# Performance work log

Measured on AMD Instinct MI355X. Metric: run time of the kernel, lower is better.

## Reference

```python
import jax, jax.numpy as jnp
import numpy as np

BN_EPS = 1e-5

def setup_inputs() -> dict:
    key = jax.random.key(0)
    ks = jax.random.split(key, 7)
    B, D, A = 16384, 768, 51
    s = 1.0 / np.sqrt(D)
    return {
        "x": jax.random.normal(ks[0], (B, D), dtype=jnp.float32),
        "W_embed": jax.random.uniform(ks[1], (D, D), minval=-s, maxval=s, dtype=jnp.float32),
        "b_embed": jax.random.uniform(ks[2], (D,), minval=-s, maxval=s, dtype=jnp.float32),
        "W_attr": jax.random.uniform(ks[3], (A, D), minval=-s, maxval=s, dtype=jnp.float32),  # stacked per-attribute (dim->1) heads
        "b_attr": jax.random.uniform(ks[4], (A,), minval=-s, maxval=s, dtype=jnp.float32),
        "gamma": jnp.ones((A,), dtype=jnp.float32),
        "beta": jnp.zeros((A,), dtype=jnp.float32),
    }

def reference(x, W_embed, b_embed, W_attr, b_attr, gamma, beta):
    # word_embed: Linear(dim, dim)
    h = x @ W_embed.T + b_embed                      # [B, D]
    # fused per-attribute heads: cat of attr_num (dim->1) linears == one (dim->attr_num) matmul
    logits = h @ W_attr.T + b_attr                    # [B, A]
    # BatchNorm1d (training mode: batch statistics, biased variance)
    mean = jnp.mean(logits, axis=0)
    var = jnp.var(logits, axis=0)
    y = (logits - mean) * jax.lax.rsqrt(var + BN_EPS) * gamma + beta
    return y
```

## Files before the change

### kernel.cpp

```cpp
#include <hip/hip_runtime.h>
#include <hip/hip_bf16.h>

typedef _Float16 halfx8 __attribute__((ext_vector_type(8)));
typedef _Float16 halfx4 __attribute__((ext_vector_type(4)));
typedef float floatx4 __attribute__((ext_vector_type(4)));

#define GLOBAL_AS __attribute__((address_space(1)))
#define LDS_AS __attribute__((address_space(3)))

__device__ __forceinline__ void async_copy_16(const void* g, void* l) {
    __builtin_amdgcn_global_load_lds((GLOBAL_AS void*)g, (LDS_AS void*)l, 16, 0, 0);
}

#define PM 16384
#define PD 768
#define PA 51


__global__ __launch_bounds__(256) void init_kernel(
    const float* __restrict__ Wa, const float* __restrict__ b_embed,
    const float* __restrict__ b_attr,
    float* __restrict__ wc32, float* __restrict__ bc, float* __restrict__ stats)
{
    int b = blockIdx.x, t = threadIdx.x;
    if (b < 12) {
        #pragma unroll
        for (int j = 0; j < 4; ++j)
            ((float4*)wc32)[b * 1024 + j * 256 + t] = (float4){0.f, 0.f, 0.f, 0.f};
    } else {
        if (t < 128) stats[t] = 0.f;
        __shared__ float red[256];
        int a = t & 63, qtr = t >> 6;
        float partial = 0.f;
        if (a < PA) {
            const float* war = Wa + (size_t)a * PD + qtr * 192;
            const float* ber = b_embed + qtr * 192;
            #pragma unroll 4
            for (int k = 0; k < 192; k += 4) {
                floatx4 w = *(const floatx4*)(war + k);
                floatx4 e = *(const floatx4*)(ber + k);
                partial += w[0]*e[0] + w[1]*e[1] + w[2]*e[2] + w[3]*e[3];
            }
        }
        red[t] = partial;
        __syncthreads();
        if (t < PA)
            bc[t] = red[t] + red[64 + t] + red[128 + t] + red[192 + t] + b_attr[t];
    }
}

__global__ __launch_bounds__(256) void wcomb_kernel(
    const float* __restrict__ We, const float* __restrict__ Wa,
    float* __restrict__ wc32)
{
    __shared__ float WeS[48 * 64];
    __shared__ float WaS[51 * 48];
    const int b = blockIdx.x;
    const int kc = b & 15;
    const int nc = b >> 4;
    const int k0 = kc * 48, d0 = nc * 64;
    const int t = threadIdx.x;

    #pragma unroll
    for (int j = 0; j < 3; ++j) {
        int idx4 = j * 256 + t;
        int r = idx4 >> 4, c4 = idx4 & 15;
        *(floatx4*)&WeS[r * 64 + c4 * 4] =
            *(const floatx4*)(We + (size_t)(k0 + r) * PD + d0 + c4 * 4);
    }
    for (int idx4 = t; idx4 < 612; idx4 += 256) {
        int r = idx4 / 12, c4 = idx4 % 12;
        *(floatx4*)&WaS[r * 48 + c4 * 4] =
            *(const floatx4*)(Wa + (size_t)r * PD + k0 + c4 * 4);
    }
    __syncthreads();

    const int c = t & 63;
    const int ag = t >> 6;

    float we[48];
    #pragma unroll
    for (int k = 0; k < 48; ++k) we[k] = WeS[k * 64 + c];

    #pragma unroll
    for (int i = 0; i < 13; ++i) {
        int a = ag + i * 4;
        if (a < PA) {
            float acc = 0.f;
            #pragma unroll
            for (int k4 = 0; k4 < 12; ++k4) {
                floatx4 wa = *(const floatx4*)&WaS[a * 48 + k4 * 4];
                acc += wa[0] * we[k4*4] + wa[1] * we[k4*4+1]
                     + wa[2] * we[k4*4+2] + wa[3] * we[k4*4+3];
            }
            atomicAdd(&wc32[(size_t)a * PD + d0 + c], acc);
        }
    }
}

__global__ __launch_bounds__(256) void skinny_gemm_kernel(
    const float* __restrict__ X,
    const float* __restrict__ Wc,
    const float* __restrict__ bc,
    float* __restrict__ logits,
    float* __restrict__ stats)
{
    __shared__ float As[32 * 64];
    __shared__ float Bs[64 * 64];
    __shared__ float s_sum[64];
    __shared__ float s_ssq[64];

    const int tid = threadIdx.x;
    const int wave = tid >> 6;
    const int lane = tid & 63;
    const int quad = lane >> 4;
    const int l16 = lane & 15;
    const int wr = wave & 1;
    const int wn = wave >> 1;
    const int row0 = blockIdx.x * 32;

    if (tid < 64) { s_sum[tid] = 0.f; s_ssq[tid] = 0.f; }

    const int g_r  = lane >> 4;
    const int g_sl = lane & 15;

    floatx4 acc[2];
    acc[0] = (floatx4){0.f, 0.f, 0.f, 0.f};
    acc[1] = (floatx4){0.f, 0.f, 0.f, 0.f};

    for (int kt = 0; kt < PD; kt += 64) {
        #pragma unroll
        for (int j = 0; j < 2; ++j) {
            int g = wave * 2 + j;
            int r = g * 4 + g_r;
            int csrc = g_sl ^ (r & 7);
            async_copy_16(X + (size_t)(row0 + r) * PD + kt + csrc * 4, &As[g * 256]);
        }
        #pragma unroll
        for (int j = 0; j < 4; ++j) {
            int g = wave * 4 + j;
            int r = g * 4 + g_r;
            int csrc = g_sl ^ (r & 7);
            async_copy_16(Wc + (size_t)r * PD + kt + csrc * 4, &Bs[g * 256]);
        }
        __syncthreads();
        #pragma unroll
        for (int ks = 0; ks < 2; ++ks) {
            int c0 = ks * 8 + quad * 2;
            int sw = l16 & 7;
            int rA = wr * 16 + l16;
            floatx4 p0 = *(const floatx4*)&As[rA * 64 + ((c0 ^ sw) << 2)];
            floatx4 p1 = *(const floatx4*)&As[rA * 64 + (((c0 + 1) ^ sw) << 2)];
            halfx8 af;
            af[0] = (_Float16)p0[0]; af[1] = (_Float16)p0[1];
            af[2] = (_Float16)p0[2]; af[3] = (_Float16)p0[3];
            af[4] = (_Float16)p1[0]; af[5] = (_Float16)p1[1];
            af[6] = (_Float16)p1[2]; af[7] = (_Float16)p1[3];
            #pragma unroll
            for (int ni = 0; ni < 2; ++ni) {
                int rB = wn * 32 + ni * 16 + l16;
                floatx4 q0 = *(const floatx4*)&Bs[rB * 64 + ((c0 ^ sw) << 2)];
                floatx4 q1 = *(const floatx4*)&Bs[rB * 64 + (((c0 + 1) ^ sw) << 2)];
                halfx8 bf;
                bf[0] = (_Float16)q0[0]; bf[1] = (_Float16)q0[1];
                bf[2] = (_Float16)q0[2]; bf[3] = (_Float16)q0[3];
                bf[4] = (_Float16)q1[0]; bf[5] = (_Float16)q1[1];
                bf[6] = (_Float16)q1[2]; bf[7] = (_Float16)q1[3];
                acc[ni] = __builtin_amdgcn_mfma_f32_16x16x32_f16(af, bf, acc[ni], 0, 0, 0);
            }
        }
        __syncthreads();
    }

    #pragma unroll
    for (int ni = 0; ni < 2; ++ni) {
        int col = wn * 32 + ni * 16 + l16;
        if (col < PA) {
            float bv = bc[col];
            float ps = 0.f, pss = 0.f;
            int rowb = row0 + wr * 16 + quad * 4;
            #pragma unroll
            for (int r = 0; r < 4; ++r) {
                float v = acc[ni][r] + bv;
                logits[(size_t)(rowb + r) * PA + col] = v;
                ps += v; pss += v * v;
            }
            atomicAdd(&s_sum[col], ps);
            atomicAdd(&s_ssq[col], pss);
        }
    }
    __syncthreads();
    if (tid < PA) {
        atomicAdd(&stats[tid], s_sum[tid]);
        atomicAdd(&stats[64 + tid], s_ssq[tid]);
    }
}

__global__ void bn_finalize_kernel(const float* __restrict__ logits,
                                   const float* __restrict__ stats,
                                   const float* __restrict__ gamma,
                                   const float* __restrict__ beta,
                                   float* __restrict__ out, int total) {
    __shared__ float s_scale[PA];
    __shared__ float s_shift[PA];
    int t = threadIdx.x;
    if (t < PA) {
        const float invB = 1.0f / (float)PM;
        float mean = stats[t] * invB;
        float var = stats[64 + t] * invB - mean * mean;
        float inv = rsqrtf(var + 1e-5f);
        float g = gamma[t] * inv;
        s_scale[t] = g;
        s_shift[t] = beta[t] - mean * g;
    }
    __syncthreads();
    int idx = blockIdx.x * 256 + t;
    if (idx < total) {
        int col = idx % PA;
        out[idx] = logits[idx] * s_scale[col] + s_shift[col];
    }
}

extern "C" void kernel_launch(void* const* d_in, const int* in_sizes, int n_in,
                              void* d_out, int out_size, void* d_ws, size_t ws_size,
                              hipStream_t stream) {
    const float* x       = (const float*)d_in[0];
    const float* W_embed = (const float*)d_in[1];
    const float* b_embed = (const float*)d_in[2];
    const float* W_attr  = (const float*)d_in[3];
    const float* b_attr  = (const float*)d_in[4];
    const float* gamma   = (const float*)d_in[5];
    const float* beta    = (const float*)d_in[6];
    float* out = (float*)d_out;

    char* ws = (char*)d_ws;
    float* wc32   = (float*)(ws);
    float* bc     = (float*)(ws + 196608);
    float* stats  = (float*)(ws + 196864);
    float* logits = (float*)(ws + 197376);

    init_kernel<<<13, 256, 0, stream>>>(W_attr, b_embed, b_attr, wc32, bc, stats);
    wcomb_kernel<<<192, 256, 0, stream>>>(W_embed, W_attr, wc32);
    skinny_gemm_kernel<<<512, 256, 0, stream>>>(x, wc32, bc, logits, stats);
    bn_finalize_kernel<<<3264, 256, 0, stream>>>(logits, stats, gamma, beta, out, PM * PA);
}
```

Before: 132.5 us.

## Fuse GEMM and BatchNorm via cooperative grid sync, merge prep kernels, double-buffer loads

```diff
diff --git a/kernel.cpp b/kernel.cpp
--- a/kernel.cpp
+++ b/kernel.cpp
@@ -1,8 +1,9 @@
 #include <hip/hip_runtime.h>
-#include <hip/hip_bf16.h>
+#include <hip/hip_cooperative_groups.h>
+
+namespace cg = cooperative_groups;
 
 typedef _Float16 halfx8 __attribute__((ext_vector_type(8)));
-typedef _Float16 halfx4 __attribute__((ext_vector_type(4)));
 typedef float floatx4 __attribute__((ext_vector_type(4)));
 
 #define GLOBAL_AS __attribute__((address_space(1)))
@@ -17,96 +18,65 @@
 #define PA 51
 
 
-__global__ __launch_bounds__(256) void init_kernel(
-    const float* __restrict__ Wa, const float* __restrict__ b_embed,
-    const float* __restrict__ b_attr,
+__global__ __launch_bounds__(256) void prep_kernel(
+    const float* __restrict__ We, const float* __restrict__ be,
+    const float* __restrict__ Wa, const float* __restrict__ ba,
     float* __restrict__ wc32, float* __restrict__ bc, float* __restrict__ stats)
 {
-    int b = blockIdx.x, t = threadIdx.x;
-    if (b < 12) {
-        #pragma unroll
-        for (int j = 0; j < 4; ++j)
-            ((float4*)wc32)[b * 1024 + j * 256 + t] = (float4){0.f, 0.f, 0.f, 0.f};
-    } else {
-        if (t < 128) stats[t] = 0.f;
-        __shared__ float red[256];
-        int a = t & 63, qtr = t >> 6;
-        float partial = 0.f;
-        if (a < PA) {
-            const float* war = Wa + (size_t)a * PD + qtr * 192;
-            const float* ber = b_embed + qtr * 192;
-            #pragma unroll 4
-            for (int k = 0; k < 192; k += 4) {
-                floatx4 w = *(const floatx4*)(war + k);
-                floatx4 e = *(const floatx4*)(ber + k);
-                partial += w[0]*e[0] + w[1]*e[1] + w[2]*e[2] + w[3]*e[3];
-            }
-        }
-        red[t] = partial;
-        __syncthreads();
-        if (t < PA)
-            bc[t] = red[t] + red[64 + t] + red[128 + t] + red[192 + t] + b_attr[t];
-    }
-}
-
-__global__ __launch_bounds__(256) void wcomb_kernel(
-    const float* __restrict__ We, const float* __restrict__ Wa,
-    float* __restrict__ wc32)
-{
-    __shared__ float WeS[48 * 64];
-    __shared__ float WaS[51 * 48];
-    const int b = blockIdx.x;
-    const int kc = b & 15;
-    const int nc = b >> 4;
-    const int k0 = kc * 48, d0 = nc * 64;
-    const int t = threadIdx.x;
-
-    #pragma unroll
-    for (int j = 0; j < 3; ++j) {
-        int idx4 = j * 256 + t;
-        int r = idx4 >> 4, c4 = idx4 & 15;
-        *(floatx4*)&WeS[r * 64 + c4 * 4] =
-            *(const floatx4*)(We + (size_t)(k0 + r) * PD + d0 + c4 * 4);
-    }
-    for (int idx4 = t; idx4 < 612; idx4 += 256) {
-        int r = idx4 / 12, c4 = idx4 % 12;
-        *(floatx4*)&WaS[r * 48 + c4 * 4] =
-            *(const floatx4*)(Wa + (size_t)r * PD + k0 + c4 * 4);
-    }
-    __syncthreads();
-
-    const int c = t & 63;
-    const int ag = t >> 6;
-
-    float we[48];
-    #pragma unroll
-    for (int k = 0; k < 48; ++k) we[k] = WeS[k * 64 + c];
-
-    #pragma unroll
-    for (int i = 0; i < 13; ++i) {
-        int a = ag + i * 4;
-        if (a < PA) {
-            float acc = 0.f;
-            #pragma unroll
-            for (int k4 = 0; k4 < 12; ++k4) {
-                floatx4 wa = *(const floatx4*)&WaS[a * 48 + k4 * 4];
-                acc += wa[0] * we[k4*4] + wa[1] * we[k4*4+1]
-                     + wa[2] * we[k4*4+2] + wa[3] * we[k4*4+3];
-            }
-            atomicAdd(&wc32[(size_t)a * PD + d0 + c], acc);
-        }
-    }
-}
-
-__global__ __launch_bounds__(256) void skinny_gemm_kernel(
+    const int wave = threadIdx.x >> 6;
+    const int lane = threadIdx.x & 63;
+    const int Wu = __builtin_amdgcn_readfirstlane((int)blockIdx.x * 4 + wave);
+
+    if (Wu < 312) {
+        const int pair = Wu / 12;
+        const int dchunk = Wu - pair * 12;
+        const int a0 = pair * 2;
+        const bool has1 = (a0 + 1 < PA);
+        const int d = dchunk * 64 + lane;
+        const float* wa0 = Wa + (size_t)a0 * PD;
+        const float* wa1 = Wa + (size_t)(has1 ? a0 + 1 : a0) * PD;
+        float acc0 = 0.f, acc1 = 0.f;
+        #pragma unroll 32
+        for (int k = 0; k < PD; ++k) {
+            float w = We[(size_t)k * PD + d];
+            acc0 = fmaf(w, wa0[k], acc0);
+            acc1 = fmaf(w, wa1[k], acc1);
+        }
+        wc32[(size_t)a0 * PD + d] = acc0;
+        if (has1) wc32[(size_t)(a0 + 1) * PD + d] = acc1;
+    } else if (Wu < 325) {
+        const int r = PA + (Wu - 312);
+        #pragma unroll
+        for (int j = 0; j < 12; ++j)
+            wc32[(size_t)r * PD + j * 64 + lane] = 0.f;
+    } else if (Wu < 376) {
+        const int a = Wu - 325;
+        float p = 0.f;
+        #pragma unroll
+        for (int j = 0; j < 12; ++j) {
+            int k = j * 64 + lane;
+            p = fmaf(Wa[(size_t)a * PD + k], be[k], p);
+        }
+        #pragma unroll
+        for (int off = 32; off; off >>= 1) p += __shfl_down(p, off);
+        if (lane == 0) bc[a] = p + ba[a];
+    } else if (Wu == 376) {
+        stats[lane] = 0.f;
+        stats[64 + lane] = 0.f;
+    }
+}
+
+__global__ void __launch_bounds__(256, 2) gemm_bn_kernel(
     const float* __restrict__ X,
     const float* __restrict__ Wc,
     const float* __restrict__ bc,
-    float* __restrict__ logits,
+    const float* __restrict__ gamma,
+    const float* __restrict__ beta,
+    float* __restrict__ out,
     float* __restrict__ stats)
 {
-    __shared__ float As[32 * 64];
-    __shared__ float Bs[64 * 64];
+    __shared__ float As[2][32 * 64];
+    __shared__ float Bs[2][64 * 64];
     __shared__ float s_sum[64];
     __shared__ float s_ssq[64];
 
@@ -117,40 +87,41 @@
     const int l16 = lane & 15;
     const int wr = wave & 1;
     const int wn = wave >> 1;
-    const int row0 = blockIdx.x * 32;
-
-    if (tid < 64) { s_sum[tid] = 0.f; s_ssq[tid] = 0.f; }
-
+    const int row0 = (int)blockIdx.x * 32;
     const int g_r  = lane >> 4;
     const int g_sl = lane & 15;
+
+    if (tid < 64) { s_sum[tid] = 0.f; s_ssq[tid] = 0.f; }
 
     floatx4 acc[2];
     acc[0] = (floatx4){0.f, 0.f, 0.f, 0.f};
     acc[1] = (floatx4){0.f, 0.f, 0.f, 0.f};
 
-    for (int kt = 0; kt < PD; kt += 64) {
+    auto stage = [&](float* AsB, float* BsB, int kt) {
         #pragma unroll
         for (int j = 0; j < 2; ++j) {
             int g = wave * 2 + j;
             int r = g * 4 + g_r;
             int csrc = g_sl ^ (r & 7);
-            async_copy_16(X + (size_t)(row0 + r) * PD + kt + csrc * 4, &As[g * 256]);
+            async_copy_16(X + (size_t)(row0 + r) * PD + kt + csrc * 4, AsB + g * 256);
         }
         #pragma unroll
         for (int j = 0; j < 4; ++j) {
             int g = wave * 4 + j;
             int r = g * 4 + g_r;
             int csrc = g_sl ^ (r & 7);
-            async_copy_16(Wc + (size_t)r * PD + kt + csrc * 4, &Bs[g * 256]);
-        }
-        __syncthreads();
+            async_copy_16(Wc + (size_t)r * PD + kt + csrc * 4, BsB + g * 256);
+        }
+    };
+
+    auto compute = [&](const float* AsB, const float* BsB) {
         #pragma unroll
         for (int ks = 0; ks < 2; ++ks) {
             int c0 = ks * 8 + quad * 2;
             int sw = l16 & 7;
             int rA = wr * 16 + l16;
-            floatx4 p0 = *(const floatx4*)&As[rA * 64 + ((c0 ^ sw) << 2)];
-            floatx4 p1 = *(const floatx4*)&As[rA * 64 + (((c0 + 1) ^ sw) << 2)];
+            floatx4 p0 = *(const floatx4*)&AsB[rA * 64 + ((c0 ^ sw) << 2)];
+            floatx4 p1 = *(const floatx4*)&AsB[rA * 64 + (((c0 + 1) ^ sw) << 2)];
             halfx8 af;
             af[0] = (_Float16)p0[0]; af[1] = (_Float16)p0[1];
             af[2] = (_Float16)p0[2]; af[3] = (_Float16)p0[3];
@@ -159,8 +130,8 @@
             #pragma unroll
             for (int ni = 0; ni < 2; ++ni) {
                 int rB = wn * 32 + ni * 16 + l16;
-                floatx4 q0 = *(const floatx4*)&Bs[rB * 64 + ((c0 ^ sw) << 2)];
-                floatx4 q1 = *(const floatx4*)&Bs[rB * 64 + (((c0 + 1) ^ sw) << 2)];
+                floatx4 q0 = *(const floatx4*)&BsB[rB * 64 + ((c0 ^ sw) << 2)];
+                floatx4 q1 = *(const floatx4*)&BsB[rB * 64 + (((c0 + 1) ^ sw) << 2)];
                 halfx8 bf;
                 bf[0] = (_Float16)q0[0]; bf[1] = (_Float16)q0[1];
                 bf[2] = (_Float16)q0[2]; bf[3] = (_Float16)q0[3];
@@ -169,20 +140,35 @@
                 acc[ni] = __builtin_amdgcn_mfma_f32_16x16x32_f16(af, bf, acc[ni], 0, 0, 0);
             }
         }
-        __syncthreads();
-    }
-
+    };
+
+    stage(As[0], Bs[0], 0);
+    #pragma unroll
+    for (int t = 0; t < 12; ++t) {
+        const int cur = t & 1;
+        if (t < 11) {
+            stage(As[cur ^ 1], Bs[cur ^ 1], (t + 1) * 64);
+            asm volatile("s_waitcnt vmcnt(6)\n\ts_barrier" ::: "memory");
+        } else {
+            asm volatile("s_waitcnt vmcnt(0)\n\ts_barrier" ::: "memory");
+        }
+        compute(As[cur], Bs[cur]);
+        asm volatile("s_waitcnt lgkmcnt(0)\n\ts_barrier" ::: "memory");
+    }
+
+    float keep[2][4];
+    int cols[2];
     #pragma unroll
     for (int ni = 0; ni < 2; ++ni) {
         int col = wn * 32 + ni * 16 + l16;
+        cols[ni] = col;
         if (col < PA) {
             float bv = bc[col];
             float ps = 0.f, pss = 0.f;
-            int rowb = row0 + wr * 16 + quad * 4;
             #pragma unroll
             for (int r = 0; r < 4; ++r) {
                 float v = acc[ni][r] + bv;
-                logits[(size_t)(rowb + r) * PA + col] = v;
+                keep[ni][r] = v;
                 ps += v; pss += v * v;
             }
             atomicAdd(&s_sum[col], ps);
@@ -194,30 +180,27 @@
         atomicAdd(&stats[tid], s_sum[tid]);
         atomicAdd(&stats[64 + tid], s_ssq[tid]);
     }
-}
-
-__global__ void bn_finalize_kernel(const float* __restrict__ logits,
-                                   const float* __restrict__ stats,
-                                   const float* __restrict__ gamma,
-                                   const float* __restrict__ beta,
-                                   float* __restrict__ out, int total) {
-    __shared__ float s_scale[PA];
-    __shared__ float s_shift[PA];
-    int t = threadIdx.x;
-    if (t < PA) {
-        const float invB = 1.0f / (float)PM;
-        float mean = stats[t] * invB;
-        float var = stats[64 + t] * invB - mean * mean;
-        float inv = rsqrtf(var + 1e-5f);
-        float g = gamma[t] * inv;
-        s_scale[t] = g;
-        s_shift[t] = beta[t] - mean * g;
-    }
-    __syncthreads();
-    int idx = blockIdx.x * 256 + t;
-    if (idx < total) {
-        int col = idx % PA;
-        out[idx] = logits[idx] * s_scale[col] + s_shift[col];
+
+    __threadfence();
+    cg::this_grid().sync();
+
+    const float invB = 1.0f / (float)PM;
+    #pragma unroll
+    for (int ni = 0; ni < 2; ++ni) {
+        int col = cols[ni];
+        if (col < PA) {
+            float s  = __hip_atomic_load(&stats[col],      __ATOMIC_RELAXED, __HIP_MEMORY_SCOPE_AGENT);
+            float ss = __hip_atomic_load(&stats[64 + col], __ATOMIC_RELAXED, __HIP_MEMORY_SCOPE_AGENT);
+            float mean = s * invB;
+            float var  = ss * invB - mean * mean;
+            float inv  = rsqrtf(var + 1e-5f);
+            float scale = gamma[col] * inv;
+            float shift = beta[col] - mean * scale;
+            int rowb = row0 + wr * 16 + quad * 4;
+            #pragma unroll
+            for (int r = 0; r < 4; ++r)
+                out[(size_t)(rowb + r) * PA + col] = keep[ni][r] * scale + shift;
+        }
     }
 }
 
@@ -234,13 +217,16 @@
     float* out = (float*)d_out;
 
     char* ws = (char*)d_ws;
-    float* wc32   = (float*)(ws);
-    float* bc     = (float*)(ws + 196608);
-    float* stats  = (float*)(ws + 196864);
-    float* logits = (float*)(ws + 197376);
-
-    init_kernel<<<13, 256, 0, stream>>>(W_attr, b_embed, b_attr, wc32, bc, stats);
-    wcomb_kernel<<<192, 256, 0, stream>>>(W_embed, W_attr, wc32);
-    skinny_gemm_kernel<<<512, 256, 0, stream>>>(x, wc32, bc, logits, stats);
-    bn_finalize_kernel<<<3264, 256, 0, stream>>>(logits, stats, gamma, beta, out, PM * PA);
-}
+    float* wc32  = (float*)(ws);
+    float* bc    = (float*)(ws + 196608);
+    float* stats = (float*)(ws + 196864);
+
+    prep_kernel<<<95, 256, 0, stream>>>(W_embed, b_embed, W_attr, b_attr, wc32, bc, stats);
+
+    void* args[] = {
+        (void*)&x, (void*)&wc32, (void*)&bc,
+        (void*)&gamma, (void*)&beta, (void*)&out, (void*)&stats
+    };
+    hipLaunchCooperativeKernel(reinterpret_cast<void*>(gemm_bn_kernel),
+                               dim3(512), dim3(256), args, 0, stream);
+}
```

Result: slower. 262.4 us (+98.0%).
